# Kernel optimization log

Measured on AMD Instinct MI355X. Metric: run time of the kernel, lower is better.

The kernel has to match this reference:

```python
import jax, jax.numpy as jnp
import numpy as np

K = 20          # neighbors
EPS = 1e-5      # InstanceNorm2d default eps
SLOPE = 0.2     # LeakyReLU negative slope


def setup_inputs() -> dict:
    key = jax.random.key(0)
    k1, k2 = jax.random.split(key)
    x = jax.random.normal(k1, (8, 64, 4096), dtype=jnp.float32)   # (B, C, N)
    W = jax.random.normal(k2, (64, 128), dtype=jnp.float32) * 0.05  # conv1x1: (C_out, 2*C_in)
    return {"x": x, "W": W}


def reference(x, W):
    B, C, N = x.shape
    xt = jnp.transpose(x, (0, 2, 1))                      # (B, N, C)
    # knn: pairwise_distance = -||xi||^2 + 2 xi.xj - ||xj||^2 (negative sq dist)
    inner = -2.0 * jnp.einsum('bcn,bcm->bnm', x, x)       # (B, N, N)
    xx = jnp.sum(x * x, axis=1)                           # (B, N)
    pd = -xx[:, :, None] - inner - xx[:, None, :]         # (B, N, N)
    idx = jax.lax.top_k(pd, K)[1]                         # (B, N, K) neighbor indices
    # gather neighbor features: (B, N, K, C)
    nbr = xt[jnp.arange(B)[:, None, None], idx]
    ctr = jnp.broadcast_to(xt[:, :, None, :], nbr.shape)  # (B, N, K, C)
    edge = jnp.concatenate([nbr - ctr, ctr], axis=-1)     # (B, N, K, 2C)
    # shared 1x1 conv (no bias): (B, O, N, K)
    y = jnp.einsum('bnkc,oc->bonk', edge, W)
    # InstanceNorm2d (affine=False): normalize each (b, o) over (N, K)
    mean = jnp.mean(y, axis=(2, 3), keepdims=True)
    var = jnp.var(y, axis=(2, 3), keepdims=True)
    y = (y - mean) * jax.lax.rsqrt(var + EPS)
    # LeakyReLU(0.2)
    y = jnp.where(y > 0, y, SLOPE * y)
    # max pool over k
    return jnp.max(y, axis=-1)                            # (B, O, N)
```

## Files before the change

kernel.cpp:

```cpp
#include <hip/hip_runtime.h>
#include <math.h>

#define B_ 8
#define C_ 64
#define N_ 4096
#define K_ 20
#define O_ 64
#define CS 8
#define NKf 81920.0f
#define EPS 1e-5f
#define SLOPE 0.2f

#define INS20(sv, mv)                                            \
  {                                                              \
    _Pragma("unroll")                                            \
    for (int j = 19; j >= 1; --j) {                              \
      bool sh = (sv) > tv[j - 1];                                \
      bool he = (!sh) && ((sv) > tv[j]);                         \
      tv[j] = sh ? tv[j - 1] : (he ? (sv) : tv[j]);              \
      ti[j] = sh ? ti[j - 1] : (he ? (mv) : ti[j]);              \
    }                                                            \
    if ((sv) > tv[0]) { tv[0] = (sv); ti[0] = (mv); }            \
  }

__global__ __launch_bounds__(256) void ka(const float* __restrict__ x,
                                          const float* __restrict__ W,
                                          float* __restrict__ xx,
                                          float* __restrict__ xT,
                                          float* __restrict__ Pt,
                                          float* __restrict__ Qt) {
  __shared__ float wl[O_ * 128];
  int t = threadIdx.x;
#pragma unroll
  for (int j = 0; j < 32; ++j) wl[t + 256 * j] = W[t + 256 * j];
  __syncthreads();
  int gid = blockIdx.x * 256 + t;
  int b = gid >> 12;
  int n = gid & 4095;
  const float* xb = x + (size_t)b * C_ * N_ + n;
  float xr[64];
  float sq = 0.f;
#pragma unroll
  for (int c = 0; c < 64; ++c) {
    xr[c] = xb[(size_t)c * N_];
    sq = fmaf(xr[c], xr[c], sq);
  }
  xx[gid] = sq;
  float* xtrow = xT + (size_t)gid * 64;
#pragma unroll
  for (int c4 = 0; c4 < 16; ++c4) {
    *(float4*)&xtrow[c4 * 4] =
        make_float4(xr[4 * c4], xr[4 * c4 + 1], xr[4 * c4 + 2], xr[4 * c4 + 3]);
  }
  float* prow = Pt + (size_t)gid * 64;
  float* qrow = Qt + (size_t)gid * 64;
  for (int o = 0; o < 64; ++o) {
    const float4* w1 = (const float4*)&wl[o * 128];
    const float4* w2 = (const float4*)&wl[o * 128 + 64];
    float pa = 0.f, pb = 0.f, qa = 0.f, qb = 0.f;
#pragma unroll
    for (int c4 = 0; c4 < 16; c4 += 2) {
      float4 wa = w1[c4], wb = w1[c4 + 1];
      float4 va = w2[c4], vb = w2[c4 + 1];
      pa = fmaf(xr[4 * c4 + 0], wa.x, pa);
      pa = fmaf(xr[4 * c4 + 1], wa.y, pa);
      pa = fmaf(xr[4 * c4 + 2], wa.z, pa);
      pa = fmaf(xr[4 * c4 + 3], wa.w, pa);
      pb = fmaf(xr[4 * c4 + 4], wb.x, pb);
      pb = fmaf(xr[4 * c4 + 5], wb.y, pb);
      pb = fmaf(xr[4 * c4 + 6], wb.z, pb);
      pb = fmaf(xr[4 * c4 + 7], wb.w, pb);
      qa = fmaf(xr[4 * c4 + 0], va.x, qa);
      qa = fmaf(xr[4 * c4 + 1], va.y, qa);
      qa = fmaf(xr[4 * c4 + 2], va.z, qa);
      qa = fmaf(xr[4 * c4 + 3], va.w, qa);
      qb = fmaf(xr[4 * c4 + 4], vb.x, qb);
      qb = fmaf(xr[4 * c4 + 5], vb.y, qb);
      qb = fmaf(xr[4 * c4 + 6], vb.z, qb);
      qb = fmaf(xr[4 * c4 + 7], vb.w, qb);
    }
    float p = pa + pb;
    prow[o] = p;
    qrow[o] = (qa + qb) - p;
  }
}

__global__ __attribute__((amdgpu_flat_work_group_size(256, 256),
                          amdgpu_waves_per_eu(2, 3)))
void kb(const float* __restrict__ xT,
        const float* __restrict__ xx,
        float* __restrict__ candv,
        int* __restrict__ candi) {
  int seg = blockIdx.x;
  int rb = blockIdx.y;
  int b = blockIdx.z;
  int t = threadIdx.x;
  int n = rb * 256 + t;
  const float* xrp = xT + ((size_t)b * N_ + n) * 64;
  float xr2[64];
#pragma unroll
  for (int c4 = 0; c4 < 16; ++c4) {
    float4 v = *(const float4*)&xrp[c4 * 4];
    xr2[4 * c4 + 0] = 2.f * v.x;
    xr2[4 * c4 + 1] = 2.f * v.y;
    xr2[4 * c4 + 2] = 2.f * v.z;
    xr2[4 * c4 + 3] = 2.f * v.w;
  }
  float tv[20];
  int ti[20];
#pragma unroll
  for (int j = 0; j < 20; ++j) { tv[j] = -INFINITY; ti[j] = 0; }
  float pv0 = 0.f, pv1 = 0.f, pv2 = 0.f, pv3 = 0.f;
  int pm0 = 0, pm1 = 0, pm2 = 0, pm3 = 0;
  int pcnt = 0;
  auto drain = [&]() {
    while (__any(pcnt > 0)) {
      bool a = pcnt > 0;
      float s2 = pv0;
      int m2 = pm0;
      if (a) {
        pv0 = pv1; pm0 = pm1;
        pv1 = pv2; pm1 = pm2;
        pv2 = pv3; pm2 = pm3;
        pcnt--;
        if (s2 > tv[19]) INS20(s2, m2);
      }
    }
  };
  const float* xcb = xT + (size_t)b * N_ * 64;
  const float* xxb = xx + (size_t)b * N_;
  const int m0 = seg * (N_ / CS);
  for (int m = m0; m < m0 + N_ / CS; ++m) {
    const float4* cp = (const float4*)(xcb + (size_t)m * 64);
    float a0 = -xxb[m], a1 = 0.f, a2 = 0.f, a3 = 0.f;
#pragma unroll
    for (int c4 = 0; c4 < 16; ++c4) {
      float4 v = cp[c4];
      a0 = fmaf(xr2[4 * c4 + 0], v.x, a0);
      a1 = fmaf(xr2[4 * c4 + 1], v.y, a1);
      a2 = fmaf(xr2[4 * c4 + 2], v.z, a2);
      a3 = fmaf(xr2[4 * c4 + 3], v.w, a3);
    }
    float s = (a0 + a1) + (a2 + a3);
    bool q = s > tv[19];
    if (__any(q)) {
      if (q) {
        pv3 = (pcnt == 3) ? s : pv3; pm3 = (pcnt == 3) ? m : pm3;
        pv2 = (pcnt == 2) ? s : pv2; pm2 = (pcnt == 2) ? m : pm2;
        pv1 = (pcnt == 1) ? s : pv1; pm1 = (pcnt == 1) ? m : pm1;
        pv0 = (pcnt == 0) ? s : pv0; pm0 = (pcnt == 0) ? m : pm0;
        pcnt++;
      }
      if (__any(pcnt == 4)) drain();
    }
  }
  drain();
  size_t base = ((size_t)(b * N_ + n) * CS + seg) * 20;
#pragma unroll
  for (int j = 0; j < 20; ++j) {
    candv[base + j] = tv[j];
    candi[base + j] = ti[j];
  }
}

__global__ __launch_bounds__(256) void kmerge(const float* __restrict__ candv,
                                              const int* __restrict__ candi,
                                              int* __restrict__ idxf) {
  int r = blockIdx.x * 256 + threadIdx.x;
  const float* cv = candv + (size_t)r * (CS * 20);
  const int* ci = candi + (size_t)r * (CS * 20);
  float tv[20];
  int ti[20];
#pragma unroll
  for (int j = 0; j < 20; ++j) { tv[j] = -INFINITY; ti[j] = 0; }
  for (int seg = 0; seg < CS; ++seg) {
    const float* cvs = cv + seg * 20;
    const int* cis = ci + seg * 20;
    for (int j = 0; j < 20; ++j) {
      float s = cvs[j];
      if (!(s > tv[19])) break;
      int m = cis[j];
      INS20(s, m);
    }
  }
  int* op = idxf + (size_t)r * 20;
#pragma unroll
  for (int j = 0; j < 20; ++j) op[j] = ti[j];
}

__global__ __launch_bounds__(256) void kd(const float* __restrict__ Pt,
                                          const float* __restrict__ Qt,
                                          const int* __restrict__ idxf,
                                          float* __restrict__ Mt,
                                          float* __restrict__ S1,
                                          float* __restrict__ S2) {
  int bi = blockIdx.x;
  int b = bi >> 8;
  int n0 = (bi & 255) * 16;
  int w = threadIdx.x >> 6;
  int o = threadIdx.x & 63;
  const float* Pb = Pt + (size_t)b * N_ * 64;
  float s1 = 0.f, s2 = 0.f;
#pragma unroll
  for (int r = 0; r < 4; ++r) {
    int n = n0 + w * 4 + r;
    const int* ip = idxf + (size_t)(b * N_ + n) * 20;
    float a = 0.f, bb = 0.f, mx = -INFINITY;
#pragma unroll
    for (int k = 0; k < 20; ++k) {
      int m = ip[k];
      float v = Pb[(size_t)m * 64 + o];
      a += v;
      bb = fmaf(v, v, bb);
      mx = fmaxf(mx, v);
    }
    float q = Qt[(size_t)(b * N_ + n) * 64 + o];
    Mt[(size_t)(b * N_ + n) * 64 + o] = mx + q;
    s1 += a + 20.f * q;
    s2 += bb + 2.f * q * a + 20.f * q * q;
  }
  __shared__ float red[8][64];
  red[w][o] = s1;
  red[4 + w][o] = s2;
  __syncthreads();
  if (threadIdx.x < 64) {
    float t1 = red[0][o] + red[1][o] + red[2][o] + red[3][o];
    float t2 = red[4][o] + red[5][o] + red[6][o] + red[7][o];
    atomicAdd(&S1[b * 64 + o], t1);
    atomicAdd(&S2[b * 64 + o], t2);
  }
}

__global__ __launch_bounds__(256) void ke(const float* __restrict__ Mt,
                                          const float* __restrict__ S1,
                                          const float* __restrict__ S2,
                                          float* __restrict__ out) {
  __shared__ float tile[64 * 65];
  __shared__ float mu[64], rs[64];
  int bi = blockIdx.x;
  int b = bi >> 6;
  int n0 = (bi & 63) * 64;
  int t = threadIdx.x;
  if (t < 64) {
    float m = S1[b * 64 + t] * (1.f / NKf);
    float v = S2[b * 64 + t] * (1.f / NKf) - m * m;
    mu[t] = m;
    rs[t] = rsqrtf(v + EPS);
  }
#pragma unroll
  for (int rr = 0; rr < 16; ++rr) {
    int f = t + rr * 256;
    int nl = f >> 6, o = f & 63;
    tile[nl * 65 + o] = Mt[((size_t)b * N_ + n0 + nl) * 64 + o];
  }
  __syncthreads();
#pragma unroll
  for (int rr = 0; rr < 16; ++rr) {
    int f = t + rr * 256;
    int o = f >> 6, nl = f & 63;
    float v = (tile[nl * 65 + o] - mu[o]) * rs[o];
    v = v > 0.f ? v : SLOPE * v;
    out[((size_t)b * 64 + o) * N_ + n0 + nl] = v;
  }
}

extern "C" void kernel_launch(void* const* d_in, const int* in_sizes, int n_in,
                              void* d_out, int out_size, void* d_ws, size_t ws_size,
                              hipStream_t stream) {
  const float* x = (const float*)d_in[0];
  const float* W = (const float*)d_in[1];
  float* out = (float*)d_out;
  float* ws = (float*)d_ws;
  float* xx = ws;
  float* xT = xx + 32768;
  float* Pt = xT + 2097152;
  float* Qt = Pt + 2097152;
  float* candv = Qt + 2097152;
  int* candi = (int*)(candv + 5242880);
  int* idxf = candi + 5242880;
  float* S1 = (float*)(idxf + 655360);
  float* S2 = S1 + 512;
  float* Mt = xT;

  hipLaunchKernelGGL(ka, dim3(128), dim3(256), 0, stream, x, W, xx, xT, Pt, Qt);
  hipLaunchKernelGGL(kb, dim3(CS, 16, 8), dim3(256), 0, stream, xT, xx, candv, candi);
  hipLaunchKernelGGL(kmerge, dim3(128), dim3(256), 0, stream, candv, candi, idxf);
  hipMemsetAsync(S1, 0, 1024 * sizeof(float), stream);
  hipLaunchKernelGGL(kd, dim3(2048), dim3(256), 0, stream, Pt, Qt, idxf, Mt, S1, S2);
  hipLaunchKernelGGL(ke, dim3(512), dim3(256), 0, stream, Mt, S1, S2, out);
}
```

Before: 864.9 us.

## Keep per-thread top-k list in shared memory with early-exit insertion

Moves the per-row 20-entry top-k candidate list in the kNN scan kernel from registers into shared memory, laid out column-wise per thread. The wave-synchronous 4-deep pending buffer and drain loop are replaced by a direct insertion sort that stops as soon as it reaches a larger element. This frees many VGPRs and the waves-per-EU hint is dropped, aiming at higher occupancy and shorter insertion paths. The cost is 40 KB of LDS per block, which may itself limit occupancy, plus LDS traffic and divergent loops within a wave.

Result: slower. 1.596 ms (+84.5%).

```diff
diff --git a/kernel.cpp b/kernel.cpp
--- a/kernel.cpp
+++ b/kernel.cpp
@@ -85,17 +85,18 @@
   }
 }
 
-__global__ __attribute__((amdgpu_flat_work_group_size(256, 256),
-                          amdgpu_waves_per_eu(2, 3)))
-void kb(const float* __restrict__ xT,
-        const float* __restrict__ xx,
-        float* __restrict__ candv,
-        int* __restrict__ candi) {
+__global__ __launch_bounds__(256) void kb(const float* __restrict__ xT,
+                                          const float* __restrict__ xx,
+                                          float* __restrict__ candv,
+                                          int* __restrict__ candi) {
+  __shared__ uint2 pr[20 * 256];
   int seg = blockIdx.x;
   int rb = blockIdx.y;
   int b = blockIdx.z;
   int t = threadIdx.x;
   int n = rb * 256 + t;
+#pragma unroll
+  for (int j = 0; j < 20; ++j) pr[j * 256 + t] = make_uint2(0xFF800000u, 0u);
   const float* xrp = xT + ((size_t)b * N_ + n) * 64;
   float xr2[64];
 #pragma unroll
@@ -106,27 +107,7 @@
     xr2[4 * c4 + 2] = 2.f * v.z;
     xr2[4 * c4 + 3] = 2.f * v.w;
   }
-  float tv[20];
-  int ti[20];
-#pragma unroll
-  for (int j = 0; j < 20; ++j) { tv[j] = -INFINITY; ti[j] = 0; }
-  float pv0 = 0.f, pv1 = 0.f, pv2 = 0.f, pv3 = 0.f;
-  int pm0 = 0, pm1 = 0, pm2 = 0, pm3 = 0;
-  int pcnt = 0;
-  auto drain = [&]() {
-    while (__any(pcnt > 0)) {
-      bool a = pcnt > 0;
-      float s2 = pv0;
-      int m2 = pm0;
-      if (a) {
-        pv0 = pv1; pm0 = pm1;
-        pv1 = pv2; pm1 = pm2;
-        pv2 = pv3; pm2 = pm3;
-        pcnt--;
-        if (s2 > tv[19]) INS20(s2, m2);
-      }
-    }
-  };
+  float rthresh = -INFINITY;
   const float* xcb = xT + (size_t)b * N_ * 64;
   const float* xxb = xx + (size_t)b * N_;
   const int m0 = seg * (N_ / CS);
@@ -142,24 +123,26 @@
       a3 = fmaf(xr2[4 * c4 + 3], v.w, a3);
     }
     float s = (a0 + a1) + (a2 + a3);
-    bool q = s > tv[19];
-    if (__any(q)) {
-      if (q) {
-        pv3 = (pcnt == 3) ? s : pv3; pm3 = (pcnt == 3) ? m : pm3;
-        pv2 = (pcnt == 2) ? s : pv2; pm2 = (pcnt == 2) ? m : pm2;
-        pv1 = (pcnt == 1) ? s : pv1; pm1 = (pcnt == 1) ? m : pm1;
-        pv0 = (pcnt == 0) ? s : pv0; pm0 = (pcnt == 0) ? m : pm0;
-        pcnt++;
+    if (s > rthresh) {
+      int j = 19;
+      while (j > 0) {
+        uint2 p = pr[(j - 1) * 256 + t];
+        if (!(__uint_as_float(p.x) < s)) break;
+        pr[j * 256 + t] = p;
+        --j;
       }
-      if (__any(pcnt == 4)) drain();
-    }
-  }
-  drain();
+      pr[j * 256 + t] = make_uint2(__float_as_uint(s), (unsigned)m);
+      rthresh = __uint_as_float(pr[19 * 256 + t].x);
+    }
+  }
   size_t base = ((size_t)(b * N_ + n) * CS + seg) * 20;
+  float* cvp = candv + base;
+  int* cip = candi + base;
 #pragma unroll
   for (int j = 0; j < 20; ++j) {
-    candv[base + j] = tv[j];
-    candi[base + j] = ti[j];
+    uint2 p = pr[j * 256 + t];
+    cvp[j] = __uint_as_float(p.x);
+    cip[j] = (int)p.y;
   }
 }
 
```
